# Optimization experiments

Measured on AMD Instinct MI355X. Metric: run time of the kernel, lower is better.

The kernel has to match this reference:

```python
import jax, jax.numpy as jnp
import numpy as np

DIM = 16
HID = 256
BATCH = 8192
N_STEPS = 10      # fixed-step RK4 replaces adaptive dopri5 for a deterministic reference
T0, T1 = 0.0, 1.0
LOG_2PI = float(np.log(2.0 * np.pi))


def setup_inputs() -> dict:
    key = jax.random.key(0)
    ks = jax.random.split(key, 7)

    def lin_w(k, fan_in, fan_out):
        lim = 1.0 / np.sqrt(fan_in)
        return jax.random.uniform(k, (fan_in, fan_out), minval=-lim, maxval=lim, dtype=jnp.float32)

    def lin_b(k, fan_in, fan_out):
        lim = 1.0 / np.sqrt(fan_in)
        return jax.random.uniform(k, (fan_out,), minval=-lim, maxval=lim, dtype=jnp.float32)

    x = jax.random.normal(ks[0], (BATCH, DIM), dtype=jnp.float32)
    return {
        "x": x,
        "W1": lin_w(ks[1], DIM + 1, HID), "b1": lin_b(ks[2], DIM + 1, HID),
        "W2": lin_w(ks[3], HID, HID),     "b2": lin_b(ks[4], HID, HID),
        "W3": lin_w(ks[5], HID, DIM),     "b3": lin_b(ks[6], HID, DIM),
    }


def _mlp(W1, b1, W2, b2, W3, b3, h):
    h = jax.nn.silu(h @ W1 + b1)
    h = jax.nn.silu(h @ W2 + b2)
    return h @ W3 + b3


def reference(x, W1, b1, W2, b2, W3, b3):
    dtype = x.dtype

    def f(t, z):  # time-conditioned vector field f(z, t): [B, d] -> [B, d]
        t_col = jnp.full((z.shape[0], 1), t, dtype=dtype)
        return _mlp(W1, b1, W2, b2, W3, b3, jnp.concatenate([z, t_col], axis=1))

    eye = jnp.eye(DIM, dtype=dtype)

    def f_and_div(t, z):
        fz = f(t, z)
        # exact divergence = trace of Jacobian, via DIM forward-mode JVPs
        def jvp_dir(e):  # e: [d]
            _, jv = jax.jvp(lambda zz: f(t, zz), (z,), (jnp.broadcast_to(e, z.shape),))
            return jv  # [B, d]
        jvs = jax.vmap(jvp_dir)(eye)          # [d, B, d]
        div = jnp.einsum('ibi->b', jvs)       # sum_i dF_i/dz_i
        return fz, div

    dt = jnp.asarray((T1 - T0) / N_STEPS, dtype=dtype)

    def rhs(t, z):
        fz, div = f_and_div(t, z)
        return fz, -div   # dz/dt, dlogp/dt

    def step(state, i):
        z, logp = state
        t = T0 + i * dt
        k1z, k1l = rhs(t, z)
        k2z, k2l = rhs(t + 0.5 * dt, z + 0.5 * dt * k1z)
        k3z, k3l = rhs(t + 0.5 * dt, z + 0.5 * dt * k2z)
        k4z, k4l = rhs(t + dt, z + dt * k3z)
        z = z + (dt / 6.0) * (k1z + 2.0 * k2z + 2.0 * k3z + k4z)
        logp = logp + (dt / 6.0) * (k1l + 2.0 * k2l + 2.0 * k3l + k4l)
        return (z, logp), None

    logp0 = jnp.zeros(x.shape[0], dtype=dtype)
    (z1, logp1), _ = jax.lax.scan(step, (x, logp0), jnp.arange(N_STEPS, dtype=dtype))

    logpz = -0.5 * (jnp.sum(z1 * z1, axis=1) + DIM * LOG_2PI)
    return logpz - logp1
```

## Files before the change

### kernel.cpp

```cpp
#include <hip/hip_runtime.h>

#define DIM 16
#define HID 256
#define NSTEPS 10
#define TILE_B 32
#define NTHR 1024
#define LSH 264

typedef __attribute__((ext_vector_type(8))) short bf16x8;
typedef __attribute__((ext_vector_type(4))) short bf16x4;
typedef __attribute__((ext_vector_type(4))) float f32x4;
typedef __attribute__((ext_vector_type(2))) float f32x2;
typedef __attribute__((ext_vector_type(2))) unsigned int u32x2;

__device__ __forceinline__ unsigned short f2bf(float f) {
    unsigned u = __float_as_uint(f);
    u += 0x7fff + ((u >> 16) & 1);
    return (unsigned short)(u >> 16);
}
__device__ __forceinline__ unsigned cvt_pk_bf16(float lo, float hi) {
    unsigned r;
    asm("v_cvt_pk_bf16_f32 %0, %1, %2" : "=v"(r) : "v"(lo), "v"(hi));
    return r;
}
__device__ __forceinline__ unsigned packtr(float a, float b) {
    return __builtin_amdgcn_perm(__float_as_uint(b), __float_as_uint(a), 0x07060302u);
}
__device__ __forceinline__ unsigned pk4_fp8(float a, float b, float c, float d) {
    int w = __builtin_amdgcn_cvt_pk_fp8_f32(a, b, 0, false);
    w = __builtin_amdgcn_cvt_pk_fp8_f32(c, d, w, true);
    return (unsigned)w;
}
__device__ __forceinline__ void silu_both(float x, float& h, float& d) {
    float s = __builtin_amdgcn_rcpf(1.0f + __expf(-x));
    h = x * s;
    d = fmaf(h, 1.0f - s, s);
}

#if defined(__has_builtin) && __has_builtin(__builtin_amdgcn_mfma_f32_16x16x16bf16_1k)
__device__ __forceinline__ f32x4 mfma16(bf16x4 a, bf16x4 b, f32x4 c) {
    return __builtin_amdgcn_mfma_f32_16x16x16bf16_1k(a, b, c, 0, 0, 0);
}
#else
__device__ __forceinline__ f32x4 mfma16(bf16x4 a, bf16x4 b, f32x4 c) {
    asm volatile("s_nop 1\n\t"
                 "v_mfma_f32_16x16x16_bf16 %0, %1, %2, %0\n\t"
                 "s_nop 7\n\t"
                 "s_nop 7"
                 : "+v"(c) : "v"(a), "v"(b));
    return c;
}
#endif

__global__ void cnf_setup(const float* __restrict__ W1, const float* __restrict__ W2,
                          const float* __restrict__ W3,
                          unsigned char* __restrict__ w2f8, unsigned char* __restrict__ mtf8) {
    const int n = blockIdx.x;
    const int j = threadIdx.x;
    float g = 0.0f;
#pragma unroll
    for (int i = 0; i < DIM; ++i) g = fmaf(W1[i * HID + j], W3[n * DIM + i], g);
    const float w2 = W2[j * HID + n];
    w2f8[n * HID + j] = (unsigned char)(__builtin_amdgcn_cvt_pk_fp8_f32(w2, w2, 0, false) & 0xff);
    const float m = w2 * g;
    mtf8[n * HID + j] = (unsigned char)(__builtin_amdgcn_cvt_pk_fp8_f32(m, m, 0, false) & 0xff);
}

__global__ __launch_bounds__(NTHR, 4) void cnf_main(
    const float* __restrict__ x,
    const float* __restrict__ W1, const float* __restrict__ b1,
    const float* __restrict__ b2, const float* __restrict__ b3,
    const unsigned char* __restrict__ w2f8, const unsigned char* __restrict__ mtf8,
    const float* __restrict__ W3, float* __restrict__ out)
{
    __shared__ unsigned short zb[TILE_B][40];
    __shared__ unsigned short w1e[HID][40];
    __shared__ unsigned short w3t[DIM][LSH];
    __shared__ unsigned char  h1f8[TILE_B][264];
    __shared__ unsigned char  d1f8[TILE_B][264];
    __shared__ unsigned char  d2f8[TILE_B][264];
    __shared__ alignas(16) float fzp[8][2][16][20];
    __shared__ alignas(16) float divp[8][TILE_B];
    __shared__ alignas(16) float b2l[HID];
    __shared__ alignas(16) float b3l[DIM];

    const int tid  = (int)threadIdx.x;
    const int lane = tid & 63;
    const int wv   = tid >> 6;
    const int g    = lane >> 4;
    const int r    = lane & 15;
    const int g8   = g * 8;
    const int b0   = (int)blockIdx.x * TILE_B;
    const int zsw  = ((r >> 3) & 1) << 3;
    const int n0w  = (wv & 7) * 32;

    float zb4[4] = {0, 0, 0, 0}, za4[4] = {0, 0, 0, 0};
    if (wv < 2) {
        const f32x4 xv = *(const f32x4*)&x[(b0 + wv * 16 + r) * DIM + 4 * g];
#pragma unroll
        for (int q = 0; q < 4; ++q) zb4[q] = xv[q];
        u32x2 pz = { cvt_pk_bf16(zb4[0], zb4[1]), cvt_pk_bf16(zb4[2], zb4[3]) };
        *(u32x2*)&zb[wv * 16 + r][(4 * g) ^ zsw] = pz;
    }
    if (tid < TILE_B) {
        const int zswi = ((tid >> 3) & 1) << 3;
#pragma unroll
        for (int c = 16; c < 32; ++c)
            zb[tid][c ^ zswi] = (c == 17) ? (unsigned short)0x3F80 : (unsigned short)0;
    }
    {
        const int n = tid >> 2, kh = (tid & 3) * 8;
#pragma unroll
        for (int e = 0; e < 8; ++e) {
            const int k = kh + e;
            float v = 0.0f;
            if (k < 17)       v = W1[k * HID + n];
            else if (k == 17) v = b1[n];
            w1e[n][k] = f2bf(v);
        }
    }
    if (tid < 512) {
        const int n = tid >> 5, k0 = (tid & 31) * 8;
#pragma unroll
        for (int j = 0; j < 8; ++j) w3t[n][k0 + j] = f2bf(W3[(k0 + j) * DIM + n]);
    }
    if (tid < HID) b2l[tid] = b2[tid];
    if (tid < DIM) b3l[tid] = b3[tid];

    __syncthreads();
    const bf16x8 w1v = *(const bf16x8*)&w1e[wv * 16 + r][g8];
    bf16x4 w3fa = {0, 0, 0, 0}, w3fb = {0, 0, 0, 0};
    if (wv < 8) {
        w3fa = *(const bf16x4*)&w3t[r][n0w + 4 * g];
        w3fb = *(const bf16x4*)&w3t[r][n0w + 16 + 4 * g];
    }

    long long breg[8][2];
    {
        const unsigned char* Bg = (wv < 8) ? w2f8 : mtf8;
#pragma unroll
        for (int k = 0; k < 8; ++k)
#pragma unroll
            for (int nt = 0; nt < 2; ++nt)
                breg[k][nt] = *(const long long*)(Bg + (n0w + nt * 16 + r) * HID + k * 32 + g8);
    }

    float lacc = 0.0f, logp = 0.0f;
    const float dt = 0.1f, dt6 = dt / 6.0f;

    for (int it = 0; it < NSTEPS * 4; ++it) {
        const int s = it & 3;
        const float wst = (s == 1 || s == 2) ? 2.0f : 1.0f;
        int opq = 0;
        asm volatile("" : "+v"(opq));
        __syncthreads();

        if (wv == 8 && lane < TILE_B && it) {
            const int ps = (it + 3) & 3;
            const float pw = (ps == 1 || ps == 2) ? 2.0f : 1.0f;
            float dv = 0.0f;
#pragma unroll
            for (int w = 0; w < 8; ++w) dv += divp[w][lane];
            lacc = fmaf(-pw, dv, lacc);
            if (ps == 3) { logp = fmaf(dt6, lacc, logp); lacc = 0.0f; }
        }

        {
            const bf16x8 bz0 = *(const bf16x8*)&zb[r][g8 ^ zsw];
            const bf16x8 bz1 = *(const bf16x8*)&zb[16 + r][g8 ^ zsw];
#pragma unroll
            for (int bt = 0; bt < 2; ++bt) {
                f32x4 c = {0.f, 0.f, 0.f, 0.f};
                c = __builtin_amdgcn_mfma_f32_16x16x32_bf16(w1v, bt ? bz1 : bz0, c, 0, 0, 0);
                float h[4], d[4];
#pragma unroll
                for (int q = 0; q < 4; ++q) silu_both(c[q], h[q], d[q]);
                const int row = bt * 16 + r;
                const int col = wv * 16 + 4 * g;
                *(unsigned*)&h1f8[row][col] = pk4_fp8(h[0], h[1], h[2], h[3]);
                *(unsigned*)&d1f8[row][col] = pk4_fp8(d[0], d[1], d[2], d[3]);
            }
        }
        __syncthreads();

        f32x4 cc[2][2];
        {
            const unsigned char (*aT)[264] = (wv < 8) ? h1f8 : d1f8;
#pragma unroll
            for (int a = 0; a < 2; ++a)
#pragma unroll
                for (int b = 0; b < 2; ++b) cc[a][b] = (f32x4){0.f, 0.f, 0.f, 0.f};
            __builtin_amdgcn_s_setprio(1);
#pragma unroll
            for (int k = 0; k < 8; ++k) {
                long long af[2];
#pragma unroll
                for (int bt = 0; bt < 2; ++bt)
                    af[bt] = *(const long long*)&aT[bt * 16 + r][k * 32 + g8];
#pragma unroll
                for (int nt = 0; nt < 2; ++nt)
#pragma unroll
                    for (int bt = 0; bt < 2; ++bt)
                        cc[nt][bt] = __builtin_amdgcn_mfma_f32_16x16x32_fp8_fp8(breg[k][nt], af[bt], cc[nt][bt], 0, 0, 0);
            }
            __builtin_amdgcn_s_setprio(0);
        }
        if (wv < 8) {
            const f32x4* bp20 = (const f32x4*)&b2l[n0w + 4 * g];
            const f32x4* bp21 = (const f32x4*)&b2l[n0w + 16 + 4 * g];
            const f32x4 bb0 = bp20[opq], bb1 = bp21[opq];
#pragma unroll
            for (int bt = 0; bt < 2; ++bt) {
                f32x4 cp = {0.f, 0.f, 0.f, 0.f};
#pragma unroll
                for (int nt = 0; nt < 2; ++nt) {
                    float h[4], d[4];
                    const f32x4 bb = nt ? bb1 : bb0;
#pragma unroll
                    for (int q = 0; q < 4; ++q) silu_both(cc[nt][bt][q] + bb[q], h[q], d[q]);
                    union { unsigned u[2]; bf16x4 v; } hb;
                    hb.u[0] = packtr(h[0], h[1]);
                    hb.u[1] = packtr(h[2], h[3]);
                    const int row = bt * 16 + r;
                    const int col = n0w + nt * 16 + 4 * g;
                    *(unsigned*)&d2f8[row][col] = pk4_fp8(d[0], d[1], d[2], d[3]);
                    cp = mfma16(nt ? w3fb : w3fa, hb.v, cp);
                }
                *(f32x4*)&fzp[wv][bt][r][4 * g] = cp;
            }
        }
        __syncthreads();

        if (wv < 2) {
            __builtin_amdgcn_s_setprio(1);
            f32x4 fa = {0.f, 0.f, 0.f, 0.f}, fb = {0.f, 0.f, 0.f, 0.f};
#pragma unroll
            for (int w = 0; w < 8; w += 2) {
                fa += *(const f32x4*)&fzp[w][wv][r][4 * g];
                fb += *(const f32x4*)&fzp[w + 1][wv][r][4 * g];
            }
            const f32x4* bp3 = (const f32x4*)&b3l[4 * g];
            const f32x4 b3v = bp3[opq];
            const float coef = (s == 2) ? dt : 0.5f * dt;
            float zn[4];
#pragma unroll
            for (int q = 0; q < 4; ++q) {
                const float fz = fa[q] + fb[q] + b3v[q];
                za4[q] = fmaf(wst, fz, za4[q]);
                if (s < 3) zn[q] = fmaf(coef, fz, zb4[q]);
                else { zb4[q] = fmaf(dt6, za4[q], zb4[q]); zn[q] = zb4[q]; za4[q] = 0.0f; }
            }
            u32x2 pz = { cvt_pk_bf16(zn[0], zn[1]), cvt_pk_bf16(zn[2], zn[3]) };
            *(u32x2*)&zb[wv * 16 + r][(4 * g) ^ zsw] = pz;
            if (wv == 0 && lane < TILE_B) {
                const int it1 = it + 1;
                const int s1 = it1 & 3;
                const float t1 = dt * (float)(it1 >> 2) + ((s1 == 0) ? 0.0f : (s1 == 3) ? dt : 0.5f * dt);
                zb[lane][16 ^ (((lane >> 3) & 1) << 3)] = f2bf(t1);
            }
            __builtin_amdgcn_s_setprio(0);
        } else if (wv >= 8) {
            float p0 = 0.0f, p1 = 0.0f;
#pragma unroll
            for (int nt = 0; nt < 2; ++nt)
#pragma unroll
                for (int bt = 0; bt < 2; ++bt) {
                    const int row = bt * 16 + r;
                    const int col = n0w + nt * 16 + 4 * g;
                    const unsigned du = *(const unsigned*)&d2f8[row][col];
                    const f32x2 lo = __builtin_amdgcn_cvt_pk_f32_fp8(du, false);
                    const f32x2 hi = __builtin_amdgcn_cvt_pk_f32_fp8(du, true);
                    float pp = (bt == 0) ? p0 : p1;
                    pp = fmaf(lo[0], cc[nt][bt][0], pp);
                    pp = fmaf(lo[1], cc[nt][bt][1], pp);
                    pp = fmaf(hi[0], cc[nt][bt][2], pp);
                    pp = fmaf(hi[1], cc[nt][bt][3], pp);
                    if (bt == 0) p0 = pp; else p1 = pp;
                }
            p0 += __shfl_xor(p0, 16, 64);
            p0 += __shfl_xor(p0, 32, 64);
            p1 += __shfl_xor(p1, 16, 64);
            p1 += __shfl_xor(p1, 32, 64);
            if (g < 2) divp[wv - 8][g * 16 + r] = g ? p1 : p0;
        }
    }

    __syncthreads();
    if (wv == 8 && lane < TILE_B) {
        float dv = 0.0f;
#pragma unroll
        for (int w = 0; w < 8; ++w) dv += divp[w][lane];
        lacc -= dv;
        logp = fmaf(dt6, lacc, logp);
        divp[0][lane] = logp;
    }
    __syncthreads();
    if (wv < 2) {
        float ss = zb4[0] * zb4[0] + zb4[1] * zb4[1] + zb4[2] * zb4[2] + zb4[3] * zb4[3];
        ss += __shfl_xor(ss, 16, 64);
        ss += __shfl_xor(ss, 32, 64);
        if (g == 0) {
            const int row = wv * 16 + r;
            out[b0 + row] = -0.5f * (ss + (float)DIM * 1.8378770664093453f) - divp[0][row];
        }
    }
}

extern "C" void kernel_launch(void* const* d_in, const int* in_sizes, int n_in,
                              void* d_out, int out_size, void* d_ws, size_t ws_size,
                              hipStream_t stream) {
    (void)in_sizes; (void)n_in; (void)out_size; (void)ws_size;
    const float* x  = (const float*)d_in[0];
    const float* W1 = (const float*)d_in[1];
    const float* b1 = (const float*)d_in[2];
    const float* W2 = (const float*)d_in[3];
    const float* b2 = (const float*)d_in[4];
    const float* W3 = (const float*)d_in[5];
    const float* b3 = (const float*)d_in[6];
    unsigned char* w2f8 = (unsigned char*)d_ws;
    unsigned char* mtf8 = w2f8 + HID * HID;

    cnf_setup<<<HID, HID, 0, stream>>>(W1, W2, W3, w2f8, mtf8);
    cnf_main<<<8192 / TILE_B, NTHR, 0, stream>>>(x, W1, b1, b2, b3, w2f8, mtf8, W3, (float*)d_out);
}
```

Baseline: 176.3 us.

## Halve batch tile and fuse value and tangent GEMMs into each wave

Shrinks the per-block batch tile from 32 to 16 rows and the block from 16 to 8 waves. Each wave now owns 32 hidden columns and computes both the W2 forward product and the tangent (M^T) product, so the divergence dot product is formed in registers instead of going through the d2f8 shared buffer. This drops one LDS buffer and its cross-wave round trip and doubles the grid size, which may improve occupancy and load balance. In exchange each wave holds twice the fp8 weight fragments in registers, and the ratio of synchronisation to MFMA work per block goes up.

```diff
diff --git a/kernel.cpp b/kernel.cpp
--- a/kernel.cpp
+++ b/kernel.cpp
@@ -3,8 +3,8 @@
 #define DIM 16
 #define HID 256
 #define NSTEPS 10
-#define TILE_B 32
-#define NTHR 1024
+#define TILE_B 16
+#define NTHR 512
 #define LSH 264
 
 typedef __attribute__((ext_vector_type(8))) short bf16x8;
@@ -78,8 +78,7 @@
     __shared__ unsigned short w3t[DIM][LSH];
     __shared__ unsigned char  h1f8[TILE_B][264];
     __shared__ unsigned char  d1f8[TILE_B][264];
-    __shared__ unsigned char  d2f8[TILE_B][264];
-    __shared__ alignas(16) float fzp[8][2][16][20];
+    __shared__ alignas(16) float fzp[8][TILE_B][20];
     __shared__ alignas(16) float divp[8][TILE_B];
     __shared__ alignas(16) float b2l[HID];
     __shared__ alignas(16) float b3l[DIM];
@@ -92,15 +91,15 @@
     const int g8   = g * 8;
     const int b0   = (int)blockIdx.x * TILE_B;
     const int zsw  = ((r >> 3) & 1) << 3;
-    const int n0w  = (wv & 7) * 32;
+    const int n0w  = wv * 32;
 
     float zb4[4] = {0, 0, 0, 0}, za4[4] = {0, 0, 0, 0};
-    if (wv < 2) {
-        const f32x4 xv = *(const f32x4*)&x[(b0 + wv * 16 + r) * DIM + 4 * g];
+    if (wv == 0) {
+        const f32x4 xv = *(const f32x4*)&x[(b0 + r) * DIM + 4 * g];
 #pragma unroll
         for (int q = 0; q < 4; ++q) zb4[q] = xv[q];
         u32x2 pz = { cvt_pk_bf16(zb4[0], zb4[1]), cvt_pk_bf16(zb4[2], zb4[3]) };
-        *(u32x2*)&zb[wv * 16 + r][(4 * g) ^ zsw] = pz;
+        *(u32x2*)&zb[r][(4 * g) ^ zsw] = pz;
     }
     if (tid < TILE_B) {
         const int zswi = ((tid >> 3) & 1) << 3;
@@ -109,9 +108,9 @@
             zb[tid][c ^ zswi] = (c == 17) ? (unsigned short)0x3F80 : (unsigned short)0;
     }
     {
-        const int n = tid >> 2, kh = (tid & 3) * 8;
-#pragma unroll
-        for (int e = 0; e < 8; ++e) {
+        const int n = tid >> 1, kh = (tid & 1) * 16;
+#pragma unroll
+        for (int e = 0; e < 16; ++e) {
             const int k = kh + e;
             float v = 0.0f;
             if (k < 17)       v = W1[k * HID + n];
@@ -119,7 +118,7 @@
             w1e[n][k] = f2bf(v);
         }
     }
-    if (tid < 512) {
+    {
         const int n = tid >> 5, k0 = (tid & 31) * 8;
 #pragma unroll
         for (int j = 0; j < 8; ++j) w3t[n][k0 + j] = f2bf(W3[(k0 + j) * DIM + n]);
@@ -128,21 +127,21 @@
     if (tid < DIM) b3l[tid] = b3[tid];
 
     __syncthreads();
-    const bf16x8 w1v = *(const bf16x8*)&w1e[wv * 16 + r][g8];
-    bf16x4 w3fa = {0, 0, 0, 0}, w3fb = {0, 0, 0, 0};
-    if (wv < 8) {
-        w3fa = *(const bf16x4*)&w3t[r][n0w + 4 * g];
-        w3fb = *(const bf16x4*)&w3t[r][n0w + 16 + 4 * g];
-    }
-
-    long long breg[8][2];
+    const bf16x8 w1v0 = *(const bf16x8*)&w1e[n0w + r][g8];
+    const bf16x8 w1v1 = *(const bf16x8*)&w1e[n0w + 16 + r][g8];
+    const bf16x4 w3f0 = *(const bf16x4*)&w3t[r][n0w + 4 * g];
+    const bf16x4 w3f1 = *(const bf16x4*)&w3t[r][n0w + 16 + 4 * g];
+
+    long long bw2[8][2], bmt[8][2];
     {
-        const unsigned char* Bg = (wv < 8) ? w2f8 : mtf8;
 #pragma unroll
         for (int k = 0; k < 8; ++k)
 #pragma unroll
-            for (int nt = 0; nt < 2; ++nt)
-                breg[k][nt] = *(const long long*)(Bg + (n0w + nt * 16 + r) * HID + k * 32 + g8);
+            for (int nt = 0; nt < 2; ++nt) {
+                const int off = (n0w + nt * 16 + r) * HID + k * 32 + g8;
+                bw2[k][nt] = *(const long long*)(w2f8 + off);
+                bmt[k][nt] = *(const long long*)(mtf8 + off);
+            }
     }
 
     float lacc = 0.0f, logp = 0.0f;
@@ -155,7 +154,7 @@
         asm volatile("" : "+v"(opq));
         __syncthreads();
 
-        if (wv == 8 && lane < TILE_B && it) {
+        if (wv == 1 && lane < TILE_B && it) {
             const int ps = (it + 3) & 3;
             const float pw = (ps == 1 || ps == 2) ? 2.0f : 1.0f;
             float dv = 0.0f;
@@ -166,78 +165,74 @@
         }
 
         {
-            const bf16x8 bz0 = *(const bf16x8*)&zb[r][g8 ^ zsw];
-            const bf16x8 bz1 = *(const bf16x8*)&zb[16 + r][g8 ^ zsw];
-#pragma unroll
-            for (int bt = 0; bt < 2; ++bt) {
+            const bf16x8 bz = *(const bf16x8*)&zb[r][g8 ^ zsw];
+#pragma unroll
+            for (int nt = 0; nt < 2; ++nt) {
                 f32x4 c = {0.f, 0.f, 0.f, 0.f};
-                c = __builtin_amdgcn_mfma_f32_16x16x32_bf16(w1v, bt ? bz1 : bz0, c, 0, 0, 0);
+                c = __builtin_amdgcn_mfma_f32_16x16x32_bf16(nt ? w1v1 : w1v0, bz, c, 0, 0, 0);
                 float h[4], d[4];
 #pragma unroll
                 for (int q = 0; q < 4; ++q) silu_both(c[q], h[q], d[q]);
-                const int row = bt * 16 + r;
-                const int col = wv * 16 + 4 * g;
-                *(unsigned*)&h1f8[row][col] = pk4_fp8(h[0], h[1], h[2], h[3]);
-                *(unsigned*)&d1f8[row][col] = pk4_fp8(d[0], d[1], d[2], d[3]);
+                const int col = n0w + nt * 16 + 4 * g;
+                *(unsigned*)&h1f8[r][col] = pk4_fp8(h[0], h[1], h[2], h[3]);
+                *(unsigned*)&d1f8[r][col] = pk4_fp8(d[0], d[1], d[2], d[3]);
             }
         }
         __syncthreads();
 
-        f32x4 cc[2][2];
+        f32x4 ch[2], cv[2];
         {
-            const unsigned char (*aT)[264] = (wv < 8) ? h1f8 : d1f8;
-#pragma unroll
-            for (int a = 0; a < 2; ++a)
-#pragma unroll
-                for (int b = 0; b < 2; ++b) cc[a][b] = (f32x4){0.f, 0.f, 0.f, 0.f};
+#pragma unroll
+            for (int nt = 0; nt < 2; ++nt) {
+                ch[nt] = (f32x4){0.f, 0.f, 0.f, 0.f};
+                cv[nt] = (f32x4){0.f, 0.f, 0.f, 0.f};
+            }
             __builtin_amdgcn_s_setprio(1);
 #pragma unroll
             for (int k = 0; k < 8; ++k) {
-                long long af[2];
-#pragma unroll
-                for (int bt = 0; bt < 2; ++bt)
-                    af[bt] = *(const long long*)&aT[bt * 16 + r][k * 32 + g8];
-#pragma unroll
-                for (int nt = 0; nt < 2; ++nt)
-#pragma unroll
-                    for (int bt = 0; bt < 2; ++bt)
-                        cc[nt][bt] = __builtin_amdgcn_mfma_f32_16x16x32_fp8_fp8(breg[k][nt], af[bt], cc[nt][bt], 0, 0, 0);
+                const long long afh = *(const long long*)&h1f8[r][k * 32 + g8];
+                const long long afd = *(const long long*)&d1f8[r][k * 32 + g8];
+#pragma unroll
+                for (int nt = 0; nt < 2; ++nt) {
+                    ch[nt] = __builtin_amdgcn_mfma_f32_16x16x32_fp8_fp8(bw2[k][nt], afh, ch[nt], 0, 0, 0);
+                    cv[nt] = __builtin_amdgcn_mfma_f32_16x16x32_fp8_fp8(bmt[k][nt], afd, cv[nt], 0, 0, 0);
+                }
             }
             __builtin_amdgcn_s_setprio(0);
         }
-        if (wv < 8) {
+        {
             const f32x4* bp20 = (const f32x4*)&b2l[n0w + 4 * g];
             const f32x4* bp21 = (const f32x4*)&b2l[n0w + 16 + 4 * g];
             const f32x4 bb0 = bp20[opq], bb1 = bp21[opq];
-#pragma unroll
-            for (int bt = 0; bt < 2; ++bt) {
-                f32x4 cp = {0.f, 0.f, 0.f, 0.f};
-#pragma unroll
-                for (int nt = 0; nt < 2; ++nt) {
-                    float h[4], d[4];
-                    const f32x4 bb = nt ? bb1 : bb0;
-#pragma unroll
-                    for (int q = 0; q < 4; ++q) silu_both(cc[nt][bt][q] + bb[q], h[q], d[q]);
-                    union { unsigned u[2]; bf16x4 v; } hb;
-                    hb.u[0] = packtr(h[0], h[1]);
-                    hb.u[1] = packtr(h[2], h[3]);
-                    const int row = bt * 16 + r;
-                    const int col = n0w + nt * 16 + 4 * g;
-                    *(unsigned*)&d2f8[row][col] = pk4_fp8(d[0], d[1], d[2], d[3]);
-                    cp = mfma16(nt ? w3fb : w3fa, hb.v, cp);
-                }
-                *(f32x4*)&fzp[wv][bt][r][4 * g] = cp;
-            }
+            f32x4 cp = {0.f, 0.f, 0.f, 0.f};
+            float pp = 0.0f;
+#pragma unroll
+            for (int nt = 0; nt < 2; ++nt) {
+                const f32x4 bb = nt ? bb1 : bb0;
+                float h[4], d[4];
+#pragma unroll
+                for (int q = 0; q < 4; ++q) silu_both(ch[nt][q] + bb[q], h[q], d[q]);
+                union { unsigned u[2]; bf16x4 v; } hb;
+                hb.u[0] = packtr(h[0], h[1]);
+                hb.u[1] = packtr(h[2], h[3]);
+                cp = mfma16(nt ? w3f1 : w3f0, hb.v, cp);
+#pragma unroll
+                for (int q = 0; q < 4; ++q) pp = fmaf(d[q], cv[nt][q], pp);
+            }
+            *(f32x4*)&fzp[wv][r][4 * g] = cp;
+            pp += __shfl_xor(pp, 16, 64);
+            pp += __shfl_xor(pp, 32, 64);
+            if (g == 0) divp[wv][r] = pp;
         }
         __syncthreads();
 
-        if (wv < 2) {
+        if (wv == 0) {
             __builtin_amdgcn_s_setprio(1);
             f32x4 fa = {0.f, 0.f, 0.f, 0.f}, fb = {0.f, 0.f, 0.f, 0.f};
 #pragma unroll
             for (int w = 0; w < 8; w += 2) {
-                fa += *(const f32x4*)&fzp[w][wv][r][4 * g];
-                fb += *(const f32x4*)&fzp[w + 1][wv][r][4 * g];
+                fa += *(const f32x4*)&fzp[w][r][4 * g];
+                fb += *(const f32x4*)&fzp[w + 1][r][4 * g];
             }
             const f32x4* bp3 = (const f32x4*)&b3l[4 * g];
             const f32x4 b3v = bp3[opq];
@@ -251,42 +246,19 @@
                 else { zb4[q] = fmaf(dt6, za4[q], zb4[q]); zn[q] = zb4[q]; za4[q] = 0.0f; }
             }
             u32x2 pz = { cvt_pk_bf16(zn[0], zn[1]), cvt_pk_bf16(zn[2], zn[3]) };
-            *(u32x2*)&zb[wv * 16 + r][(4 * g) ^ zsw] = pz;
-            if (wv == 0 && lane < TILE_B) {
+            *(u32x2*)&zb[r][(4 * g) ^ zsw] = pz;
+            if (lane < TILE_B) {
                 const int it1 = it + 1;
                 const int s1 = it1 & 3;
                 const float t1 = dt * (float)(it1 >> 2) + ((s1 == 0) ? 0.0f : (s1 == 3) ? dt : 0.5f * dt);
                 zb[lane][16 ^ (((lane >> 3) & 1) << 3)] = f2bf(t1);
             }
             __builtin_amdgcn_s_setprio(0);
-        } else if (wv >= 8) {
-            float p0 = 0.0f, p1 = 0.0f;
-#pragma unroll
-            for (int nt = 0; nt < 2; ++nt)
-#pragma unroll
-                for (int bt = 0; bt < 2; ++bt) {
-                    const int row = bt * 16 + r;
-                    const int col = n0w + nt * 16 + 4 * g;
-                    const unsigned du = *(const unsigned*)&d2f8[row][col];
-                    const f32x2 lo = __builtin_amdgcn_cvt_pk_f32_fp8(du, false);
-                    const f32x2 hi = __builtin_amdgcn_cvt_pk_f32_fp8(du, true);
-                    float pp = (bt == 0) ? p0 : p1;
-                    pp = fmaf(lo[0], cc[nt][bt][0], pp);
-                    pp = fmaf(lo[1], cc[nt][bt][1], pp);
-                    pp = fmaf(hi[0], cc[nt][bt][2], pp);
-                    pp = fmaf(hi[1], cc[nt][bt][3], pp);
-                    if (bt == 0) p0 = pp; else p1 = pp;
-                }
-            p0 += __shfl_xor(p0, 16, 64);
-            p0 += __shfl_xor(p0, 32, 64);
-            p1 += __shfl_xor(p1, 16, 64);
-            p1 += __shfl_xor(p1, 32, 64);
-            if (g < 2) divp[wv - 8][g * 16 + r] = g ? p1 : p0;
         }
     }
 
     __syncthreads();
-    if (wv == 8 && lane < TILE_B) {
+    if (wv == 1 && lane < TILE_B) {
         float dv = 0.0f;
 #pragma unroll
         for (int w = 0; w < 8; ++w) dv += divp[w][lane];
@@ -295,14 +267,12 @@
         divp[0][lane] = logp;
     }
     __syncthreads();
-    if (wv < 2) {
+    if (wv == 0) {
         float ss = zb4[0] * zb4[0] + zb4[1] * zb4[1] + zb4[2] * zb4[2] + zb4[3] * zb4[3];
         ss += __shfl_xor(ss, 16, 64);
         ss += __shfl_xor(ss, 32, 64);
-        if (g == 0) {
-            const int row = wv * 16 + r;
-            out[b0 + row] = -0.5f * (ss + (float)DIM * 1.8378770664093453f) - divp[0][row];
-        }
+        if (g == 0)
+            out[b0 + r] = -0.5f * (ss + (float)DIM * 1.8378770664093453f) - divp[0][r];
     }
 }
 
```

New measurement: 186.7 us. 5.9% more time.
